# Performance work log

Measured on AMD Instinct MI355X. Metric: run time of the kernel, lower is better.

Reference implementation:

```python
import jax, jax.numpy as jnp
import numpy as np

N_EMBD = 1024
N_HEAD = 16
HEAD_SIZE = 64
BLOCK_SIZE = 2048


def setup_inputs() -> dict:
    key = jax.random.key(0)
    ks = jax.random.split(key, 5)
    B, T = 2, 2048
    s_attn = 1.0 / np.sqrt(N_EMBD)
    x = jax.random.normal(ks[0], (B, T, N_EMBD), dtype=jnp.float32)
    W_attn = jax.random.normal(ks[1], (N_EMBD, 3 * N_EMBD), dtype=jnp.float32) * s_attn
    b_attn = jnp.zeros((3 * N_EMBD,), dtype=jnp.float32)
    W_proj = jax.random.normal(ks[2], (N_EMBD, N_EMBD), dtype=jnp.float32) * s_attn
    b_proj = jnp.zeros((N_EMBD,), dtype=jnp.float32)
    return {"x": x, "W_attn": W_attn, "b_attn": b_attn, "W_proj": W_proj, "b_proj": b_proj}


def reference(x, W_attn, b_attn, W_proj, b_proj):
    B, T, C = x.shape
    H, D = N_HEAD, HEAD_SIZE
    qkv = x @ W_attn + b_attn                      # [B, T, 3C]
    q, k, v = jnp.split(qkv, 3, axis=-1)
    # [B, H, T, D]
    q = q.reshape(B, T, H, D).transpose(0, 2, 1, 3)
    k = k.reshape(B, T, H, D).transpose(0, 2, 1, 3)
    v = v.reshape(B, T, H, D).transpose(0, 2, 1, 3)
    scores = jnp.einsum("bhqd,bhkd->bhqk", q, k) / jnp.sqrt(jnp.float32(D))
    causal = jnp.tril(jnp.ones((T, T), dtype=bool))
    scores = jnp.where(causal[None, None, :, :], scores, -jnp.inf)
    weights = jax.nn.softmax(scores, axis=-1)
    attn = jnp.einsum("bhqk,bhkd->bhqd", weights, v)  # [B, H, T, D]
    attn = attn.transpose(0, 2, 1, 3).reshape(B, T, C)
    return attn @ W_proj + b_proj
```

## Files before the change

### kernel.cpp

```cpp
#include <hip/hip_runtime.h>
#include <hip/hip_bf16.h>

#define NE 1024
#define NH 16
#define HD 64
#define TSEQ 2048
#define BATCH 2
#define MB (1024u * 1024u)

typedef __attribute__((ext_vector_type(8))) short bf16x8;
typedef __attribute__((ext_vector_type(4))) float f32x4;
typedef __attribute__((ext_vector_type(4))) unsigned int u32x4;
typedef unsigned short u16;
typedef unsigned int u32;

__device__ inline u16 f2bf(float f) {
    __hip_bfloat16 h = __float2bfloat16(f);
    return *reinterpret_cast<u16*>(&h);
}

__device__ inline float bf2f(u32 bits) {
    u32 v = bits << 16;
    return __builtin_bit_cast(float, v);
}

__device__ inline u32 cvt_pk_bf16(float lo, float hi) {
    u32 r;
    asm("v_cvt_pk_bf16_f32 %0, %1, %2" : "=v"(r) : "v"(lo), "v"(hi));
    return r;
}

#define GLD16(gptr, lptr)                                                        \
    __builtin_amdgcn_global_load_lds(                                            \
        (const __attribute__((address_space(1))) void*)(gptr),                   \
        (__attribute__((address_space(3))) void*)(lptr), 16, 0, 0)

__global__ void k_f32_to_bf16(const float* __restrict__ in, u16* __restrict__ out, int n4) {
    int i = blockIdx.x * blockDim.x + threadIdx.x;
    int stride = gridDim.x * blockDim.x;
    for (; i < n4; i += stride) {
        float4 v = reinterpret_cast<const float4*>(in)[i];
        ushort4 o;
        o.x = f2bf(v.x); o.y = f2bf(v.y); o.z = f2bf(v.z); o.w = f2bf(v.w);
        reinterpret_cast<ushort4*>(out)[i] = o;
    }
}

__global__ void k_prep_w(const float* __restrict__ Wa, const float* __restrict__ Wp,
                         u16* __restrict__ WaT, u16* __restrict__ WpT) {
    __shared__ float tile[32][33];
    const bool isA = blockIdx.x < 96;
    const float* in = isA ? Wa : Wp;
    u16* out = isA ? WaT : WpT;
    const int N = isA ? 3 * NE : NE;
    const int K = NE;
    int bn = (isA ? blockIdx.x : blockIdx.x - 96) * 32;
    int bk = blockIdx.y * 32;
    int tx = threadIdx.x, ty = threadIdx.y;
#pragma unroll
    for (int i = 0; i < 32; i += 8)
        tile[ty + i][tx] = in[(size_t)(bk + ty + i) * N + bn + tx];
    __syncthreads();
#pragma unroll
    for (int i = 0; i < 32; i += 8)
        out[(size_t)(bn + ty + i) * K + bk + tx] = f2bf(tile[tx][ty + i]);
}

template <int MODE>
__global__ __launch_bounds__(256, 2) void k_gemm_bt(
    const u16* __restrict__ A, const u16* __restrict__ Bt,
    const float* __restrict__ bias, void* __restrict__ outp,
    int M, int N, int K) {
    __shared__ __align__(16) u16 As[2][128 * 32];
    __shared__ __align__(16) u16 Bs[2][128 * 32];
    const int l = threadIdx.x & 63;
    const int w = threadIdx.x >> 6;
    const int m0 = blockIdx.x * 128;
    const int n0 = blockIdx.y * 128;
    const int wr = w >> 1, wc = w & 1;
    const int srow = l >> 2;
    const int scol = (l & 3) * 8;

    f32x4 acc[4][4] = {};
    const int nkt = K >> 5;

#pragma unroll
    for (int i = 0; i < 2; ++i) {
        int c = w * 2 + i;
        GLD16(A + (size_t)(m0 + c * 16 + srow) * K + scol, &As[0][c * 512]);
        GLD16(Bt + (size_t)(n0 + c * 16 + srow) * K + scol, &Bs[0][c * 512]);
    }
    __syncthreads();

    int cur = 0;
    for (int kt = 0; kt < nkt; ++kt) {
        if (kt + 1 < nkt) {
            int nb = cur ^ 1;
            int kc = ((kt + 1) << 5) + scol;
#pragma unroll
            for (int i = 0; i < 2; ++i) {
                int c = w * 2 + i;
                GLD16(A + (size_t)(m0 + c * 16 + srow) * K + kc, &As[nb][c * 512]);
                GLD16(Bt + (size_t)(n0 + c * 16 + srow) * K + kc, &Bs[nb][c * 512]);
            }
        }
        bf16x8 af[4], bfr[4];
#pragma unroll
        for (int mi = 0; mi < 4; ++mi)
            af[mi] = *reinterpret_cast<const bf16x8*>(
                &As[cur][(wr * 64 + mi * 16 + (l & 15)) * 32 + (l >> 4) * 8]);
#pragma unroll
        for (int ni = 0; ni < 4; ++ni)
            bfr[ni] = *reinterpret_cast<const bf16x8*>(
                &Bs[cur][(wc * 64 + ni * 16 + (l & 15)) * 32 + (l >> 4) * 8]);
#pragma unroll
        for (int mi = 0; mi < 4; ++mi)
#pragma unroll
            for (int ni = 0; ni < 4; ++ni)
                acc[mi][ni] = __builtin_amdgcn_mfma_f32_16x16x32_bf16(af[mi], bfr[ni], acc[mi][ni], 0, 0, 0);
        __syncthreads();
        cur ^= 1;
    }

    if (MODE == 1) {
        float* C = (float*)outp;
#pragma unroll
        for (int mi = 0; mi < 4; ++mi)
#pragma unroll
            for (int ni = 0; ni < 4; ++ni) {
                int n = n0 + wc * 64 + ni * 16 + (l & 15);
                float bv = bias[n];
#pragma unroll
                for (int r = 0; r < 4; ++r) {
                    int m = m0 + wr * 64 + mi * 16 + (l >> 4) * 4 + r;
                    C[(size_t)m * N + n] = acc[mi][ni][r] + bv;
                }
            }
    } else {
        u16* qkv = (u16*)outp;
        const size_t headsz = (size_t)BATCH * NH * TSEQ * HD;
#pragma unroll
        for (int mi = 0; mi < 4; ++mi)
#pragma unroll
            for (int ni = 0; ni < 4; ++ni) {
                int n = n0 + wc * 64 + ni * 16 + (l & 15);
                float bv = bias[n];
                int which = n >> 10;
                int c = n & 1023;
                int h = c >> 6, d = c & 63;
#pragma unroll
                for (int r = 0; r < 4; ++r) {
                    int m = m0 + wr * 64 + mi * 16 + (l >> 4) * 4 + r;
                    int b = m >> 11, t = m & 2047;
                    float v = acc[mi][ni][r] + bv;
                    size_t dst;
                    if (which == 2)
                        dst = 2 * headsz + ((size_t)(b * NH + h) * HD + d) * TSEQ + t;
                    else
                        dst = (size_t)which * headsz + ((size_t)(b * NH + h) * TSEQ + t) * HD + d;
                    qkv[dst] = f2bf(v);
                }
            }
    }
}

__global__ __launch_bounds__(256, 4) void k_attn(
    const u16* __restrict__ qb, const u16* __restrict__ kb, const u16* __restrict__ vtb,
    u16* __restrict__ oPart, float* __restrict__ mlPart) {
    __shared__ __align__(16) u16 Ks[2][64 * 64];
    __shared__ __align__(16) u16 Vs[2][64 * 64];
    const int l = threadIdx.x & 63;
    const int w = threadIdx.x >> 6;
    const int g = l >> 4, l15 = l & 15;

    const int bid = blockIdx.x;
    const int t = 15 - (bid >> 6);
    const int half = (bid >> 5) & 1;
    const int bh = bid & 31;
    const int q0 = t * 128;
    const int ktLo = half ? (t + 1) : 0;
    const int ktHi = half ? (2 * t + 2) : (t + 1);

    const size_t base = (size_t)bh * TSEQ * HD;
    const u16* Q = qb + base;
    const u16* Kg = kb + base;
    const u16* Vg = vtb + base;

    const int lrow8 = l >> 3;
    const int lchunk = (l & 7) ^ lrow8;

    const int qrow0 = q0 + w * 32 + l15;
    const int qrow1 = qrow0 + 16;
    bf16x8 qa[2][2];
#pragma unroll
    for (int ks = 0; ks < 2; ++ks) {
        qa[0][ks] = *reinterpret_cast<const bf16x8*>(Q + (size_t)qrow0 * HD + ks * 32 + g * 8);
        qa[1][ks] = *reinterpret_cast<const bf16x8*>(Q + (size_t)qrow1 * HD + ks * 32 + g * 8);
    }

    float m[2] = {0.f, 0.f};
    f32x4 o[2][4] = {};
    f32x4 os[2] = {};

    const float SC = 0.125f * 1.44269504f;
    const float THRU = 44.3614f;

    const int srcA = ((2 * g) & 3) * 16 + l15;
    const int srcB = ((2 * g + 1) & 3) * 16 + l15;
    const bool losel = (g < 2);

    u32x4 onesw = {0x3F803F80u, 0x3F803F80u, 0x3F803F80u, 0x3F803F80u};
    const bf16x8 onesA = __builtin_bit_cast(bf16x8, onesw);

#pragma unroll
    for (int i2 = 0; i2 < 2; ++i2) {
        int c = w * 2 + i2;
        GLD16(Kg + (size_t)(ktLo * 64 + c * 8 + lrow8) * HD + lchunk * 8, &Ks[0][c * 512]);
        GLD16(Vg + (size_t)(c * 8 + lrow8) * TSEQ + ktLo * 64 + lchunk * 8, &Vs[0][c * 512]);
    }
    __syncthreads();

    int cur = 0;
    for (int kt = ktLo; kt < ktHi; ++kt) {
        if (kt + 1 < ktHi) {
            int nb = cur ^ 1;
#pragma unroll
            for (int i2 = 0; i2 < 2; ++i2) {
                int c = w * 2 + i2;
                GLD16(Kg + (size_t)((kt + 1) * 64 + c * 8 + lrow8) * HD + lchunk * 8,
                      &Ks[nb][c * 512]);
                GLD16(Vg + (size_t)(c * 8 + lrow8) * TSEQ + (kt + 1) * 64 + lchunk * 8,
                      &Vs[nb][c * 512]);
            }
        }
        const u16* Kc = Ks[cur];
        const u16* Vc = Vs[cur];

        f32x4 s[4][2] = {};
        __builtin_amdgcn_s_setprio(1);
#pragma unroll
        for (int f = 0; f < 4; ++f)
#pragma unroll
            for (int ks = 0; ks < 2; ++ks) {
                bf16x8 bk = *reinterpret_cast<const bf16x8*>(
                    Kc + (f * 16 + l15) * 64 + (((ks * 4 + g) ^ (l15 & 7)) * 8));
                s[f][0] = __builtin_amdgcn_mfma_f32_16x16x32_bf16(bk, qa[0][ks], s[f][0], 0, 0, 0);
                s[f][1] = __builtin_amdgcn_mfma_f32_16x16x32_bf16(bk, qa[1][ks], s[f][1], 0, 0, 0);
            }
        __builtin_amdgcn_s_setprio(0);

        if (kt >= 2 * t) {
#pragma unroll
            for (int f = 0; f < 4; ++f)
#pragma unroll
                for (int r = 0; r < 4; ++r) {
                    int kg = (kt << 6) + f * 16 + g * 4 + r;
                    if (kg > qrow0) s[f][0][r] = -1e30f;
                    if (kg > qrow1) s[f][1][r] = -1e30f;
                }
        }

        u32 pk0[2][4], pk1[2][4];
#pragma unroll
        for (int qn = 0; qn < 2; ++qn) {
            float rmax = -1e30f;
#pragma unroll
            for (int f = 0; f < 4; ++f)
                rmax = fmaxf(rmax, fmaxf(fmaxf(s[f][qn][0], s[f][qn][1]),
                                         fmaxf(s[f][qn][2], s[f][qn][3])));
            rmax = fmaxf(rmax, __shfl_xor(rmax, 16));
            rmax = fmaxf(rmax, __shfl_xor(rmax, 32));

            if (__any(rmax - m[qn] > THRU)) {
                float mnew = fmaxf(m[qn], rmax);
                float alpha = exp2f((m[qn] - mnew) * SC);
                m[qn] = mnew;
#pragma unroll
                for (int r = 0; r < 4; ++r)
                    os[qn][r] *= alpha;
#pragma unroll
                for (int nf = 0; nf < 4; ++nf)
#pragma unroll
                    for (int r = 0; r < 4; ++r)
                        o[qn][nf][r] *= alpha;
            }
            const float mc = m[qn] * SC;
#pragma unroll
            for (int f = 0; f < 4; ++f) {
                float p0 = exp2f(__builtin_fmaf(s[f][qn][0], SC, -mc));
                float p1 = exp2f(__builtin_fmaf(s[f][qn][1], SC, -mc));
                float p2 = exp2f(__builtin_fmaf(s[f][qn][2], SC, -mc));
                float p3 = exp2f(__builtin_fmaf(s[f][qn][3], SC, -mc));
                pk0[qn][f] = cvt_pk_bf16(p0, p1);
                pk1[qn][f] = cvt_pk_bf16(p2, p3);
            }
        }

        __builtin_amdgcn_s_setprio(1);
#pragma unroll
        for (int ks = 0; ks < 2; ++ks) {
            bf16x8 pb[2];
#pragma unroll
            for (int qn = 0; qn < 2; ++qn) {
                u32 t00 = (u32)__shfl((int)pk0[qn][2 * ks], srcA);
                u32 t01 = (u32)__shfl((int)pk0[qn][2 * ks + 1], srcA);
                u32 t10 = (u32)__shfl((int)pk1[qn][2 * ks], srcA);
                u32 t11 = (u32)__shfl((int)pk1[qn][2 * ks + 1], srcA);
                u32 t20 = (u32)__shfl((int)pk0[qn][2 * ks], srcB);
                u32 t21 = (u32)__shfl((int)pk0[qn][2 * ks + 1], srcB);
                u32 t30 = (u32)__shfl((int)pk1[qn][2 * ks], srcB);
                u32 t31 = (u32)__shfl((int)pk1[qn][2 * ks + 1], srcB);
                u32x4 bb;
                bb.x = losel ? t00 : t01;
                bb.y = losel ? t10 : t11;
                bb.z = losel ? t20 : t21;
                bb.w = losel ? t30 : t31;
                pb[qn] = __builtin_bit_cast(bf16x8, bb);
            }
            os[0] = __builtin_amdgcn_mfma_f32_16x16x32_bf16(onesA, pb[0], os[0], 0, 0, 0);
            os[1] = __builtin_amdgcn_mfma_f32_16x16x32_bf16(onesA, pb[1], os[1], 0, 0, 0);
#pragma unroll
            for (int nf = 0; nf < 4; ++nf) {
                bf16x8 bv = *reinterpret_cast<const bf16x8*>(
                    Vc + (nf * 16 + l15) * 64 + (((ks * 4 + g) ^ (l15 & 7)) * 8));
                o[0][nf] = __builtin_amdgcn_mfma_f32_16x16x32_bf16(bv, pb[0], o[0][nf], 0, 0, 0);
                o[1][nf] = __builtin_amdgcn_mfma_f32_16x16x32_bf16(bv, pb[1], o[1][nf], 0, 0, 0);
            }
        }
        __builtin_amdgcn_s_setprio(0);
        __syncthreads();
        cur ^= 1;
    }

    const size_t oHalf = (size_t)32 * TSEQ * HD;
#pragma unroll
    for (int qn = 0; qn < 2; ++qn) {
        int qrow = qn ? qrow1 : qrow0;
        u16* oRow = oPart + half * oHalf + ((size_t)bh * TSEQ + qrow) * HD;
#pragma unroll
        for (int nf = 0; nf < 4; ++nf) {
            int d0 = nf * 16 + g * 4;
            u32 p01 = cvt_pk_bf16(o[qn][nf][0], o[qn][nf][1]);
            u32 p23 = cvt_pk_bf16(o[qn][nf][2], o[qn][nf][3]);
            *reinterpret_cast<u32*>(oRow + d0) = p01;
            *reinterpret_cast<u32*>(oRow + d0 + 2) = p23;
        }
        if (g == 0) {
            float* mlH = mlPart + half * ((size_t)32 * 2 * TSEQ);
            mlH[((size_t)bh * 2 + 0) * TSEQ + qrow] = m[qn];
            mlH[((size_t)bh * 2 + 1) * TSEQ + qrow] = os[qn][0];
        }
    }
}

__global__ void k_merge(const u16* __restrict__ oPart, const float* __restrict__ mlPart,
                        u16* __restrict__ attn_out) {
    const float SC = 0.125f * 1.44269504f;
    int tid = blockIdx.x * blockDim.x + threadIdx.x;
    int dblk = tid & 7;
    int q = (tid >> 3) & 2047;
    int bh = tid >> 14;
    const size_t oHalf = (size_t)32 * TSEQ * HD;
    const size_t mlHalf = (size_t)32 * 2 * TSEQ;
    float mA = mlPart[((size_t)bh * 2 + 0) * TSEQ + q];
    float lA = mlPart[((size_t)bh * 2 + 1) * TSEQ + q];
    float mB = mlPart[mlHalf + ((size_t)bh * 2 + 0) * TSEQ + q];
    float lB = mlPart[mlHalf + ((size_t)bh * 2 + 1) * TSEQ + q];
    float M = fmaxf(mA, mB);
    float eA = exp2f((mA - M) * SC);
    float eB = exp2f((mB - M) * SC);
    float invL = 1.0f / (lA * eA + lB * eB);
    float fA = eA * invL, fB = eB * invL;
    const u32* pa = (const u32*)(oPart + ((size_t)bh * TSEQ + q) * HD + dblk * 8);
    const u32* pb = (const u32*)(oPart + oHalf + ((size_t)bh * TSEQ + q) * HD + dblk * 8);
    u32 outw[4];
#pragma unroll
    for (int i = 0; i < 4; ++i) {
        u32 a = pa[i], b = pb[i];
        float lo = bf2f(a & 0xffffu) * fA + bf2f(b & 0xffffu) * fB;
        float hi = bf2f(a >> 16) * fA + bf2f(b >> 16) * fB;
        outw[i] = cvt_pk_bf16(lo, hi);
    }
    int bb = bh >> 4, h = bh & 15;
    u16* dst = attn_out + ((size_t)(bb * TSEQ + q) * NE) + h * HD + dblk * 8;
    *reinterpret_cast<u32x4*>(dst) = *reinterpret_cast<const u32x4*>(outw);
}

extern "C" void kernel_launch(void* const* d_in, const int* in_sizes, int n_in,
                              void* d_out, int out_size, void* d_ws, size_t ws_size,
                              hipStream_t stream) {
    const float* x = (const float*)d_in[0];
    const float* W_attn = (const float*)d_in[1];
    const float* b_attn = (const float*)d_in[2];
    const float* W_proj = (const float*)d_in[3];
    const float* b_proj = (const float*)d_in[4];
    float* out = (float*)d_out;

    char* ws = (char*)d_ws;
    u16* xb     = (u16*)(ws);
    u16* WaT    = (u16*)(ws + 8 * MB);
    u16* qkvb   = (u16*)(ws + 16 * MB);
    u16* WpT    = (u16*)(ws + 40 * MB);
    float* mlP  = (float*)(ws + 42 * MB);
    u16* oPart  = (u16*)(ws);
    u16* attn   = (u16*)(ws + 16 * MB);

    const int M = BATCH * TSEQ;

    k_f32_to_bf16<<<2048, 256, 0, stream>>>(x, xb, (M * NE) / 4);
    k_prep_w<<<dim3(128, NE / 32), dim3(32, 8), 0, stream>>>(W_attn, W_proj, WaT, WpT);

    k_gemm_bt<0><<<dim3(M / 128, (3 * NE) / 128), 256, 0, stream>>>(xb, WaT, b_attn, qkvb, M, 3 * NE, NE);

    const size_t headsz = (size_t)BATCH * NH * TSEQ * HD;
    k_attn<<<dim3(16 * 2 * 32), 256, 0, stream>>>(qkvb, qkvb + headsz, qkvb + 2 * headsz, oPart, mlP);

    k_merge<<<dim3((32 * TSEQ * 8) / 256), 256, 0, stream>>>(oPart, mlP, attn);

    k_gemm_bt<1><<<dim3(M / 128, NE / 128), 256, 0, stream>>>(attn, WpT, b_proj, out, M, NE, NE);
}
```

Before: 124.9 us.

## Widen GEMM K-tile to 64 with XOR-swizzled LDS and reorder attention tile schedule

The GEMM kernel now stages 64-wide K slices instead of 32, halving the number of loop iterations and barriers, and stores rows in LDS with an XOR chunk swizzle to avoid bank conflicts on fragment reads. LDS usage doubles to 64 KB per block, which may limit occupancy under the launch bound of 2. Separately, the attention kernel's query-tile order changes from strictly descending to a snake pattern across groups of four. The intent is to balance causal work across concurrently resident blocks.

```diff
diff --git a/kernel.cpp b/kernel.cpp
--- a/kernel.cpp
+++ b/kernel.cpp
@@ -71,56 +71,64 @@
     const u16* __restrict__ A, const u16* __restrict__ Bt,
     const float* __restrict__ bias, void* __restrict__ outp,
     int M, int N, int K) {
-    __shared__ __align__(16) u16 As[2][128 * 32];
-    __shared__ __align__(16) u16 Bs[2][128 * 32];
+    __shared__ __align__(16) u16 As[2][128 * 64];
+    __shared__ __align__(16) u16 Bs[2][128 * 64];
     const int l = threadIdx.x & 63;
     const int w = threadIdx.x >> 6;
     const int m0 = blockIdx.x * 128;
     const int n0 = blockIdx.y * 128;
     const int wr = w >> 1, wc = w & 1;
-    const int srow = l >> 2;
-    const int scol = (l & 3) * 8;
+    const int l15 = l & 15, g = l >> 4;
+    const int lrow8 = l >> 3;
+    const int lchunk = (l & 7) ^ lrow8;
 
     f32x4 acc[4][4] = {};
-    const int nkt = K >> 5;
-
-#pragma unroll
-    for (int i = 0; i < 2; ++i) {
-        int c = w * 2 + i;
-        GLD16(A + (size_t)(m0 + c * 16 + srow) * K + scol, &As[0][c * 512]);
-        GLD16(Bt + (size_t)(n0 + c * 16 + srow) * K + scol, &Bs[0][c * 512]);
-    }
+    const int nkt = K >> 6;
+
+#define GEMM_STAGE(buf, kbase)                                                    \
+    {                                                                             \
+        _Pragma("unroll")                                                         \
+        for (int i2 = 0; i2 < 4; ++i2) {                                          \
+            int c = w * 4 + i2;                                                   \
+            GLD16(A + (size_t)(m0 + c * 8 + lrow8) * K + (kbase) + lchunk * 8,    \
+                  &As[buf][c * 512]);                                             \
+            GLD16(Bt + (size_t)(n0 + c * 8 + lrow8) * K + (kbase) + lchunk * 8,   \
+                  &Bs[buf][c * 512]);                                             \
+        }                                                                         \
+    }
+
+    GEMM_STAGE(0, 0);
     __syncthreads();
 
     int cur = 0;
     for (int kt = 0; kt < nkt; ++kt) {
-        if (kt + 1 < nkt) {
-            int nb = cur ^ 1;
-            int kc = ((kt + 1) << 5) + scol;
-#pragma unroll
-            for (int i = 0; i < 2; ++i) {
-                int c = w * 2 + i;
-                GLD16(A + (size_t)(m0 + c * 16 + srow) * K + kc, &As[nb][c * 512]);
-                GLD16(Bt + (size_t)(n0 + c * 16 + srow) * K + kc, &Bs[nb][c * 512]);
-            }
-        }
-        bf16x8 af[4], bfr[4];
-#pragma unroll
-        for (int mi = 0; mi < 4; ++mi)
-            af[mi] = *reinterpret_cast<const bf16x8*>(
-                &As[cur][(wr * 64 + mi * 16 + (l & 15)) * 32 + (l >> 4) * 8]);
-#pragma unroll
-        for (int ni = 0; ni < 4; ++ni)
-            bfr[ni] = *reinterpret_cast<const bf16x8*>(
-                &Bs[cur][(wc * 64 + ni * 16 + (l & 15)) * 32 + (l >> 4) * 8]);
-#pragma unroll
-        for (int mi = 0; mi < 4; ++mi)
-#pragma unroll
-            for (int ni = 0; ni < 4; ++ni)
-                acc[mi][ni] = __builtin_amdgcn_mfma_f32_16x16x32_bf16(af[mi], bfr[ni], acc[mi][ni], 0, 0, 0);
+        if (kt + 1 < nkt)
+            GEMM_STAGE(cur ^ 1, (kt + 1) << 6);
+#pragma unroll
+        for (int ks2 = 0; ks2 < 2; ++ks2) {
+            bf16x8 af[4], bfr[4];
+#pragma unroll
+            for (int mi = 0; mi < 4; ++mi) {
+                int row = wr * 64 + mi * 16 + l15;
+                af[mi] = *reinterpret_cast<const bf16x8*>(
+                    &As[cur][row * 64 + (((ks2 * 4 + g) ^ (row & 7)) * 8)]);
+            }
+#pragma unroll
+            for (int ni = 0; ni < 4; ++ni) {
+                int row = wc * 64 + ni * 16 + l15;
+                bfr[ni] = *reinterpret_cast<const bf16x8*>(
+                    &Bs[cur][row * 64 + (((ks2 * 4 + g) ^ (row & 7)) * 8)]);
+            }
+#pragma unroll
+            for (int mi = 0; mi < 4; ++mi)
+#pragma unroll
+                for (int ni = 0; ni < 4; ++ni)
+                    acc[mi][ni] = __builtin_amdgcn_mfma_f32_16x16x32_bf16(af[mi], bfr[ni], acc[mi][ni], 0, 0, 0);
+        }
         __syncthreads();
         cur ^= 1;
     }
+#undef GEMM_STAGE
 
     if (MODE == 1) {
         float* C = (float*)outp;
@@ -128,11 +136,11 @@
         for (int mi = 0; mi < 4; ++mi)
 #pragma unroll
             for (int ni = 0; ni < 4; ++ni) {
-                int n = n0 + wc * 64 + ni * 16 + (l & 15);
+                int n = n0 + wc * 64 + ni * 16 + l15;
                 float bv = bias[n];
 #pragma unroll
                 for (int r = 0; r < 4; ++r) {
-                    int m = m0 + wr * 64 + mi * 16 + (l >> 4) * 4 + r;
+                    int m = m0 + wr * 64 + mi * 16 + g * 4 + r;
                     C[(size_t)m * N + n] = acc[mi][ni][r] + bv;
                 }
             }
@@ -143,14 +151,14 @@
         for (int mi = 0; mi < 4; ++mi)
 #pragma unroll
             for (int ni = 0; ni < 4; ++ni) {
-                int n = n0 + wc * 64 + ni * 16 + (l & 15);
+                int n = n0 + wc * 64 + ni * 16 + l15;
                 float bv = bias[n];
                 int which = n >> 10;
                 int c = n & 1023;
                 int h = c >> 6, d = c & 63;
 #pragma unroll
                 for (int r = 0; r < 4; ++r) {
-                    int m = m0 + wr * 64 + mi * 16 + (l >> 4) * 4 + r;
+                    int m = m0 + wr * 64 + mi * 16 + g * 4 + r;
                     int b = m >> 11, t = m & 2047;
                     float v = acc[mi][ni][r] + bv;
                     size_t dst;
@@ -174,7 +182,9 @@
     const int g = l >> 4, l15 = l & 15;
 
     const int bid = blockIdx.x;
-    const int t = 15 - (bid >> 6);
+    const int i = bid >> 6;
+    const int k4 = i >> 2, a4 = i & 3;
+    const int t = 4 * k4 + ((k4 & 1) ? (3 - a4) : a4);
     const int half = (bid >> 5) & 1;
     const int bh = bid & 31;
     const int q0 = t * 128;
```

Result: slower. 135.6 us (+8.5%).
